# Kernel optimization log

Hardware: AMD Instinct MI355X
Metric: run time of the kernel (lower is better)

## Reference

```python
import jax, jax.numpy as jnp
import numpy as np

EPS = 1e-5  # torch LayerNorm default eps

def _mish(x):
    return x * jnp.tanh(jax.nn.softplus(x))

def _ln(x, g, b):
    mu = jnp.mean(x, axis=-1, keepdims=True)
    var = jnp.mean(jnp.square(x - mu), axis=-1, keepdims=True)
    return (x - mu) * jax.lax.rsqrt(var + EPS) * g + b

def setup_inputs() -> dict:
    key = jax.random.key(0)
    ks = jax.random.split(key, 10)
    B, D, O1, O2, O3 = 65536, 784, 512, 264, 128
    def lin(k, fan_in, shape):
        bound = 1.0 / np.sqrt(fan_in)
        return jax.random.uniform(k, shape, jnp.float32, -bound, bound)
    return {
        "x":  jax.random.uniform(ks[0], (B, D), jnp.float32),
        "W1": lin(ks[1], D,  (O1, D)),   # enFC1, bias=False
        "g1": jnp.ones((O1,), jnp.float32), "b1": jnp.zeros((O1,), jnp.float32),
        "W2": lin(ks[2], O1, (O2, O1)),  # enFC2, bias=False
        "g2": jnp.ones((O2,), jnp.float32), "b2": jnp.zeros((O2,), jnp.float32),
        "W3": lin(ks[3], O2, (O3, O2)),  # enFC3 with bias
        "b3": lin(ks[4], O2, (O3,)),
        "gh": jnp.ones((O3,), jnp.float32), "bh": jnp.zeros((O3,), jnp.float32),
        "D1": lin(ks[5], O3, (O2, O3)),  # deFC1, bias=False
        "g3": jnp.ones((O2,), jnp.float32), "b3n": jnp.zeros((O2,), jnp.float32),
        "D2": lin(ks[6], O2, (O1, O2)),  # deFC2, bias=False
        "g4": jnp.ones((O1,), jnp.float32), "b4": jnp.zeros((O1,), jnp.float32),
        "D3": lin(ks[7], O1, (D, O1)),   # deFC3 with bias
        "bo": lin(ks[8], O1, (D,)),
    }

def reference(x, W1, g1, b1, W2, g2, b2, W3, b3, gh, bh,
              D1, g3, b3n, D2, g4, b4, D3, bo):
    h = _mish(_ln(x @ W1.T, g1, b1))
    h = _mish(_ln(h @ W2.T, g2, b2))
    x_latent = _mish(_ln(h @ W3.T + b3, gh, bh))
    h = _mish(_ln(x_latent @ D1.T, g3, b3n))
    h = _mish(_ln(h @ D2.T, g4, b4))
    out = jax.nn.sigmoid(h @ D3.T + bo)
    return out, jnp.sum(jnp.abs(x_latent))
```

## Files before the change

kernel.cpp:

```cpp
#include <hip/hip_runtime.h>


typedef short bf16x8 __attribute__((ext_vector_type(8)));
typedef float f32x4  __attribute__((ext_vector_type(4)));

#define B_ROWS 65536
#define EPS_LN 1e-5f

static __device__ __forceinline__ unsigned short f2bf(float f) {
    union { float f; unsigned u; } v; v.f = f;
    unsigned r = v.u + 0x7FFFu + ((v.u >> 16) & 1u);
    return (unsigned short)(r >> 16);
}

static __device__ __forceinline__ float mish_f(float x) {
    if (x > 15.f) return x;
    float u = __expf(x);
    float p = __fmaf_rn(u, u, 2.f * u);
    return x * (p / (p + 2.f));
}

static __device__ __forceinline__ void glds16(const void* g, void* l) {
    typedef __attribute__((address_space(3))) unsigned lds_u32;
    typedef __attribute__((address_space(1))) const unsigned glb_u32;
    lds_u32* lp = (lds_u32*)l;
    unsigned lofs = __builtin_amdgcn_readfirstlane((unsigned)(unsigned long long)lp);
    lp = (lds_u32*)(unsigned long long)lofs;
    __builtin_amdgcn_global_load_lds((glb_u32*)g, lp, 16, 0, 0);
}

struct CvtArgs {
    const float* src[6];
    unsigned short* dst[6];
    int O[6], K[6], KP[6];
    int base[7];
};

__global__ void wpad_kernel(CvtArgs a) {
    int b = blockIdx.x;
    int seg = 0;
    while (b >= a.base[seg + 1]) ++seg;
    int r = b - a.base[seg];
    int O = a.O[seg], K = a.K[seg], KP = a.KP[seg];
    const float* s = a.src[seg];
    unsigned short* d = a.dst[seg];
    for (int c = threadIdx.x; c < KP; c += 256) {
        unsigned short v = 0;
        if (r < O && c < K) v = f2bf(s[(size_t)r * K + c]);
        d[(size_t)r * KP + c] = v;
    }
}

template<int KP, int ASTR, int BN, int OREAL, int OSTRIDE, int NKT,
         bool SRCF32, bool HASBIAS, bool ABS, bool LN, bool SWAPGRID>
__global__ __launch_bounds__(512, 2)
void layer9(const void* __restrict__ Asrc,
            const unsigned short* __restrict__ Wp,
            const float* __restrict__ gam,
            const float* __restrict__ bet,
            const float* __restrict__ bias,
            void* __restrict__ Aout,
            float* __restrict__ partials)
{
    constexpr int NT   = BN / 64;
    constexpr int NCHW = BN / 8;
    constexpr int NCH  = NCHW + (SRCF32 ? 0 : 16);
    constexpr int MAXC = (NCH + 7) / 8;
    constexpr int ABY  = 128 * 128;
    constexpr int WBY  = BN * 128;

    __shared__ __align__(16) char smem[2 * ABY + 2 * WBY];

    const int tid  = threadIdx.x;
    const int lane = tid & 63;
    const int wu   = __builtin_amdgcn_readfirstlane(tid >> 6);
    const int wr = wu >> 2, wc = wu & 3;
    const int lg = lane >> 4, lc = lane & 15;
    const int row0  = (SWAPGRID ? blockIdx.y : blockIdx.x) * 128;
    const int cbase = LN ? 0 : (SWAPGRID ? blockIdx.x : blockIdx.y) * BN;

    const int crow = lane >> 3;
    const int sg   = (lane & 7) ^ crow;
    const size_t vofW = ((size_t)crow * KP + (size_t)(sg << 3)) * 2;
    const size_t vofA = ((size_t)crow * ASTR + (size_t)(sg << 3)) * 2;

    auto stage = [&](int t, int b) {
#pragma unroll
        for (int i = 0; i < MAXC; ++i) {
            int c = wu + 8 * i;
            if (c < NCHW) {
                const char* g = (const char*)Wp +
                    ((size_t)(cbase + c * 8) * KP) * 2 + (size_t)t * 128 + vofW;
                glds16(g, smem + (2 * ABY + b * WBY + c * 1024));
            } else if (c < NCH) {
                int ca = c - NCHW;
                const char* g = (const char*)Asrc +
                    ((size_t)(row0 + ca * 8) * ASTR) * 2 + (size_t)t * 128 + vofA;
                glds16(g, smem + (b * ABY + ca * 1024));
            }
        }
    };

    const int ar = tid >> 2, as = tid & 3;
    const float* axp = (const float*)Asrc + (size_t)(row0 + ar) * ASTR + as * 16;
    float4 rA[4];
#pragma unroll
    for (int j = 0; j < 4; ++j) rA[j] = make_float4(0, 0, 0, 0);

    auto loadA1 = [&](int t) {
#pragma unroll
        for (int j = 0; j < 4; ++j) {
            int c0 = t * 64 + as * 16 + j * 4;
            rA[j] = (c0 + 3 < 784) ? *(const float4*)(axp + t * 64 + j * 4)
                                   : make_float4(0, 0, 0, 0);
        }
    };
    auto pubA = [&](int b) {
        union { unsigned short us[8]; uint4 v; } u0, u1;
        u0.us[0] = f2bf(rA[0].x); u0.us[1] = f2bf(rA[0].y);
        u0.us[2] = f2bf(rA[0].z); u0.us[3] = f2bf(rA[0].w);
        u0.us[4] = f2bf(rA[1].x); u0.us[5] = f2bf(rA[1].y);
        u0.us[6] = f2bf(rA[1].z); u0.us[7] = f2bf(rA[1].w);
        u1.us[0] = f2bf(rA[2].x); u1.us[1] = f2bf(rA[2].y);
        u1.us[2] = f2bf(rA[2].z); u1.us[3] = f2bf(rA[2].w);
        u1.us[4] = f2bf(rA[3].x); u1.us[5] = f2bf(rA[3].y);
        u1.us[6] = f2bf(rA[3].z); u1.us[7] = f2bf(rA[3].w);
        int s0 = as * 2, rb = b * ABY + ar * 128, rx = ar & 7;
        *(uint4*)(smem + rb + (((s0    ) ^ rx) << 4)) = u0.v;
        *(uint4*)(smem + rb + (((s0 + 1) ^ rx) << 4)) = u1.v;
    };

    stage(0, 0);
    if constexpr (SRCF32) { loadA1(0); pubA(0); }
    __syncthreads();

    f32x4 acc[4][NT];
#pragma unroll
    for (int a = 0; a < 4; ++a)
#pragma unroll
        for (int c = 0; c < NT; ++c) acc[a][c] = (f32x4){0.f, 0.f, 0.f, 0.f};

    const int f0 = ((lg ^ (lc & 7)) << 4);

    for (int t = 0; t < NKT; ++t) {
        const int bsel = t & 1;
        if (t + 1 < NKT) {
            stage(t + 1, bsel ^ 1);
            if constexpr (SRCF32) loadA1(t + 1);
        }
        const char* Ab = smem + bsel * ABY + (wr * 64 + lc) * 128;
        const char* Bb = smem + 2 * ABY + bsel * WBY + (wc * NT * 16 + lc) * 128;
#pragma unroll
        for (int h = 0; h < 2; ++h) {
            const int fh = f0 ^ (h << 6);
            bf16x8 afr[4], bfr[NT];
#pragma unroll
            for (int a = 0; a < 4; ++a)
                afr[a] = *(const bf16x8*)(Ab + a * 2048 + fh);
#pragma unroll
            for (int c = 0; c < NT; ++c)
                bfr[c] = *(const bf16x8*)(Bb + c * 2048 + fh);
            __builtin_amdgcn_s_setprio(1);
#pragma unroll
            for (int c = 0; c < NT; ++c)
#pragma unroll
                for (int a = 0; a < 4; ++a)
                    acc[a][c] = __builtin_amdgcn_mfma_f32_16x16x32_bf16(afr[a], bfr[c], acc[a][c], 0, 0, 0);
            __builtin_amdgcn_s_setprio(0);
        }
        if constexpr (SRCF32) { if (t + 1 < NKT) pubA(bsel ^ 1); }
        __syncthreads();
    }

    if constexpr (LN) {
        if constexpr (HASBIAS) {
#pragma unroll
            for (int c = 0; c < NT; ++c) {
                int col = wc * NT * 16 + c * 16 + lc;
                float bv = (col < OREAL) ? bias[col] : 0.f;
#pragma unroll
                for (int a = 0; a < 4; ++a)
#pragma unroll
                    for (int r = 0; r < 4; ++r) acc[a][c][r] += bv;
            }
        }
        float ps1[4][4], ps2[4][4];
#pragma unroll
        for (int a = 0; a < 4; ++a)
#pragma unroll
            for (int r = 0; r < 4; ++r) { ps1[a][r] = 0.f; ps2[a][r] = 0.f; }
#pragma unroll
        for (int a = 0; a < 4; ++a)
#pragma unroll
            for (int c = 0; c < NT; ++c)
#pragma unroll
                for (int r = 0; r < 4; ++r) {
                    float v = acc[a][c][r];
                    ps1[a][r] += v;
                    ps2[a][r] = __fmaf_rn(v, v, ps2[a][r]);
                }
#pragma unroll
        for (int m = 1; m < 16; m <<= 1)
#pragma unroll
            for (int a = 0; a < 4; ++a)
#pragma unroll
                for (int r = 0; r < 4; ++r) {
                    ps1[a][r] += __shfl_xor(ps1[a][r], m);
                    ps2[a][r] += __shfl_xor(ps2[a][r], m);
                }

        float* lnP  = (float*)smem;
        float* lnMR = (float*)(smem + 4096);
        float* wsum = (float*)(smem + 5120);

        if (lc == 0) {
#pragma unroll
            for (int a = 0; a < 4; ++a)
#pragma unroll
                for (int r = 0; r < 4; ++r) {
                    int row = wr * 64 + a * 16 + lg * 4 + r;
                    lnP[row * 4 + wc]       = ps1[a][r];
                    lnP[512 + row * 4 + wc] = ps2[a][r];
                }
        }
        __syncthreads();
        if (tid < 128) {
            float s1 = lnP[tid * 4] + lnP[tid * 4 + 1] + lnP[tid * 4 + 2] + lnP[tid * 4 + 3];
            float s2 = lnP[512 + tid * 4] + lnP[512 + tid * 4 + 1] +
                       lnP[512 + tid * 4 + 2] + lnP[512 + tid * 4 + 3];
            float mu = s1 * (1.f / OREAL);
            float var = fmaxf(s2 * (1.f / OREAL) - mu * mu, 0.f);
            lnMR[tid]       = mu;
            lnMR[128 + tid] = rsqrtf(var + EPS_LN);
        }
        __syncthreads();

        float gcol[NT], bcol[NT];
#pragma unroll
        for (int c = 0; c < NT; ++c) {
            int col = wc * NT * 16 + c * 16 + lc;
            gcol[c] = (col < OREAL) ? gam[col] : 0.f;
            bcol[c] = (col < OREAL) ? bet[col] : 0.f;
        }

        float asum = 0.f;
        unsigned short* outp = (unsigned short*)Aout;
#pragma unroll
        for (int a = 0; a < 4; ++a)
#pragma unroll
            for (int r = 0; r < 4; ++r) {
                int rl = wr * 64 + a * 16 + lg * 4 + r;
                float mu = lnMR[rl], rs = lnMR[128 + rl];
                size_t rowoff = (size_t)(row0 + rl) * OSTRIDE;
#pragma unroll
                for (int c = 0; c < NT; ++c) {
                    int col = wc * NT * 16 + c * 16 + lc;
                    if (col < OSTRIDE) {
                        unsigned short outv = 0;
                        if (col < OREAL) {
                            float v = (acc[a][c][r] - mu) * rs * gcol[c] + bcol[c];
                            float mz = mish_f(v);
                            if (ABS) asum += fabsf(mz);
                            outv = f2bf(mz);
                        }
                        outp[rowoff + col] = outv;
                    }
                }
            }

        if constexpr (ABS) {
#pragma unroll
            for (int m = 1; m < 64; m <<= 1) asum += __shfl_xor(asum, m);
            if (lane == 0) wsum[wu] = asum;
            __syncthreads();
            if (tid == 0) {
                float s = 0.f;
                for (int w = 0; w < 8; ++w) s += wsum[w];
                partials[blockIdx.x] = s;
            }
        }
    } else {
        float* outp = (float*)Aout;
#pragma unroll
        for (int c = 0; c < NT; ++c) {
            int col = cbase + wc * NT * 16 + c * 16 + lc;
            bool ok = col < OREAL;
            float bv = ok ? bias[col] : 0.f;
#pragma unroll
            for (int a = 0; a < 4; ++a)
#pragma unroll
                for (int r = 0; r < 4; ++r) {
                    if (ok) {
                        int rl = wr * 64 + a * 16 + lg * 4 + r;
                        float v = acc[a][c][r] + bv;
                        outp[(size_t)(row0 + rl) * OSTRIDE + col] = 1.f / (1.f + __expf(-v));
                    }
                }
        }
    }
}

__global__ __launch_bounds__(512, 2)
void trio(const unsigned short* __restrict__ actP,
          const unsigned short* __restrict__ W2p,
          const unsigned short* __restrict__ W3p,
          const unsigned short* __restrict__ D1p,
          const float* __restrict__ g2, const float* __restrict__ b2,
          const float* __restrict__ gh, const float* __restrict__ bh,
          const float* __restrict__ b3,
          const float* __restrict__ g3, const float* __restrict__ b3n,
          unsigned short* __restrict__ actQ,
          float* __restrict__ partials)
{
    __shared__ __align__(16) char smem[139264];

    const int tid  = threadIdx.x;
    const int lane = tid & 63;
    const int wu   = __builtin_amdgcn_readfirstlane(tid >> 6);
    const int wr = wu >> 2, wc = wu & 3;
    const int lg = lane >> 4, lc = lane & 15;
    const int row0 = blockIdx.x * 128;

    const int sgl = (lane & 3) ^ ((lane >> 3) & 3);
    const size_t vofA  = ((size_t)(lane >> 2) * 512 + (size_t)(sgl << 3)) * 2;
    const size_t vofW2 = vofA;
    const size_t vofW3 = ((size_t)(lane >> 2) * 288 + (size_t)(sgl << 3)) * 2;
    const size_t vofD1 = ((size_t)(lane >> 2) * 128 + (size_t)(sgl << 3)) * 2;

    const int fswz = ((lg ^ ((lc >> 1) & 3)) << 4);

    float* lnP  = (float*)smem;
    float* lnMR = (float*)(smem + 4096);
    float* wsum = (float*)(smem + 5120);

    auto ln_stats = [&](float ps1[4][4], float ps2[4][4], float invO) {
#pragma unroll
        for (int m = 1; m < 16; m <<= 1)
#pragma unroll
            for (int a = 0; a < 4; ++a)
#pragma unroll
                for (int r = 0; r < 4; ++r) {
                    ps1[a][r] += __shfl_xor(ps1[a][r], m);
                    ps2[a][r] += __shfl_xor(ps2[a][r], m);
                }
        if (lc == 0) {
#pragma unroll
            for (int a = 0; a < 4; ++a)
#pragma unroll
                for (int r = 0; r < 4; ++r) {
                    int row = wr * 64 + a * 16 + lg * 4 + r;
                    lnP[row * 4 + wc]       = ps1[a][r];
                    lnP[512 + row * 4 + wc] = ps2[a][r];
                }
        }
        __syncthreads();
        if (tid < 128) {
            float s1 = lnP[tid * 4] + lnP[tid * 4 + 1] + lnP[tid * 4 + 2] + lnP[tid * 4 + 3];
            float s2 = lnP[512 + tid * 4] + lnP[512 + tid * 4 + 1] +
                       lnP[512 + tid * 4 + 2] + lnP[512 + tid * 4 + 3];
            float mu = s1 * invO;
            float var = fmaxf(s2 * invO - mu * mu, 0.f);
            lnMR[tid]       = mu;
            lnMR[128 + tid] = rsqrtf(var + EPS_LN);
        }
        __syncthreads();
    };

    {
        constexpr int NT = 6;
        f32x4 acc[4][NT];
#pragma unroll
        for (int a = 0; a < 4; ++a)
#pragma unroll
            for (int c = 0; c < NT; ++c) acc[a][c] = (f32x4){0.f, 0.f, 0.f, 0.f};

        auto stage1 = [&](int t, int b) {
#pragma unroll
            for (int i = 0; i < 4; ++i) {
                int c = wu + 8 * i;
                if (c < 24) {
                    const char* g = (const char*)W2p +
                        ((size_t)(c * 16) * 512) * 2 + (size_t)t * 64 + vofW2;
                    glds16(g, smem + (16384 + b * 24576 + c * 1024));
                } else {
                    int ca = c - 24;
                    const char* g = (const char*)actP +
                        ((size_t)(row0 + ca * 16) * 512) * 2 + (size_t)t * 64 + vofA;
                    glds16(g, smem + (b * 8192 + ca * 1024));
                }
            }
        };

        stage1(0, 0);
        __syncthreads();
        for (int t = 0; t < 16; ++t) {
            const int bsel = t & 1;
            if (t + 1 < 16) stage1(t + 1, bsel ^ 1);
            const char* Ab = smem + bsel * 8192 + (wr * 64 + lc) * 64 + fswz;
            const char* Bb = smem + 16384 + bsel * 24576 + (wc * 96 + lc) * 64 + fswz;
            bf16x8 afr[4], bfr[NT];
#pragma unroll
            for (int a = 0; a < 4; ++a) afr[a] = *(const bf16x8*)(Ab + a * 1024);
#pragma unroll
            for (int c = 0; c < NT; ++c) bfr[c] = *(const bf16x8*)(Bb + c * 1024);
            __builtin_amdgcn_s_setprio(1);
#pragma unroll
            for (int c = 0; c < NT; ++c)
#pragma unroll
                for (int a = 0; a < 4; ++a)
                    acc[a][c] = __builtin_amdgcn_mfma_f32_16x16x32_bf16(afr[a], bfr[c], acc[a][c], 0, 0, 0);
            __builtin_amdgcn_s_setprio(0);
            __syncthreads();
        }

        float ps1[4][4], ps2[4][4];
#pragma unroll
        for (int a = 0; a < 4; ++a)
#pragma unroll
            for (int r = 0; r < 4; ++r) { ps1[a][r] = 0.f; ps2[a][r] = 0.f; }
#pragma unroll
        for (int a = 0; a < 4; ++a)
#pragma unroll
            for (int c = 0; c < NT; ++c)
#pragma unroll
                for (int r = 0; r < 4; ++r) {
                    float v = acc[a][c][r];
                    ps1[a][r] += v;
                    ps2[a][r] = __fmaf_rn(v, v, ps2[a][r]);
                }
        ln_stats(ps1, ps2, 1.f / 264);

        float gcol[NT], bcol[NT];
#pragma unroll
        for (int c = 0; c < NT; ++c) {
            int col = wc * 96 + c * 16 + lc;
            gcol[c] = (col < 264) ? g2[col] : 0.f;
            bcol[c] = (col < 264) ? b2[col] : 0.f;
        }
#pragma unroll
        for (int a = 0; a < 4; ++a)
#pragma unroll
            for (int r = 0; r < 4; ++r) {
                int rl = wr * 64 + a * 16 + lg * 4 + r;
                float mu = lnMR[rl], rs = lnMR[128 + rl];
                int sx = (rl >> 1) & 3;
                int rowb = 65536 + rl * 576;
#pragma unroll
                for (int c = 0; c < NT; ++c) {
                    int col = wc * 96 + c * 16 + lc;
                    if (col < 288) {
                        unsigned short outv = 0;
                        if (col < 264) {
                            float v = (acc[a][c][r] - mu) * rs * gcol[c] + bcol[c];
                            outv = f2bf(mish_f(v));
                        }
                        int byte = rowb + ((col >> 5) << 6) +
                                   ((((col >> 3) & 3) ^ sx) << 4) + ((col & 7) << 1);
                        *(unsigned short*)(smem + byte) = outv;
                    }
                }
            }
        __syncthreads();
    }

    {
        constexpr int NT = 2;
        f32x4 acc[4][NT];
#pragma unroll
        for (int a = 0; a < 4; ++a)
#pragma unroll
            for (int c = 0; c < NT; ++c) acc[a][c] = (f32x4){0.f, 0.f, 0.f, 0.f};

        auto stage2 = [&](int t, int b) {
            int c = wu;
            const char* g = (const char*)W3p +
                ((size_t)(c * 16) * 288) * 2 + (size_t)t * 64 + vofW3;
            glds16(g, smem + (b * 8192 + c * 1024));
        };

        stage2(0, 0);
        __syncthreads();
        for (int t = 0; t < 9; ++t) {
            const int bsel = t & 1;
            if (t + 1 < 9) stage2(t + 1, bsel ^ 1);
            const char* Ab = smem + 65536 + (wr * 64 + lc) * 576 + t * 64 + fswz;
            const char* Bb = smem + bsel * 8192 + (wc * 32 + lc) * 64 + fswz;
            bf16x8 afr[4], bfr[NT];
#pragma unroll
            for (int a = 0; a < 4; ++a) afr[a] = *(const bf16x8*)(Ab + a * 16 * 576);
#pragma unroll
            for (int c = 0; c < NT; ++c) bfr[c] = *(const bf16x8*)(Bb + c * 1024);
            __builtin_amdgcn_s_setprio(1);
#pragma unroll
            for (int c = 0; c < NT; ++c)
#pragma unroll
                for (int a = 0; a < 4; ++a)
                    acc[a][c] = __builtin_amdgcn_mfma_f32_16x16x32_bf16(afr[a], bfr[c], acc[a][c], 0, 0, 0);
            __builtin_amdgcn_s_setprio(0);
            __syncthreads();
        }

#pragma unroll
        for (int c = 0; c < NT; ++c) {
            int col = wc * 32 + c * 16 + lc;
            float bv = b3[col];
#pragma unroll
            for (int a = 0; a < 4; ++a)
#pragma unroll
                for (int r = 0; r < 4; ++r) acc[a][c][r] += bv;
        }
        float ps1[4][4], ps2[4][4];
#pragma unroll
        for (int a = 0; a < 4; ++a)
#pragma unroll
            for (int r = 0; r < 4; ++r) { ps1[a][r] = 0.f; ps2[a][r] = 0.f; }
#pragma unroll
        for (int a = 0; a < 4; ++a)
#pragma unroll
            for (int c = 0; c < NT; ++c)
#pragma unroll
                for (int r = 0; r < 4; ++r) {
                    float v = acc[a][c][r];
                    ps1[a][r] += v;
                    ps2[a][r] = __fmaf_rn(v, v, ps2[a][r]);
                }
        ln_stats(ps1, ps2, 1.f / 128);

        float gcol[NT], bcol[NT];
#pragma unroll
        for (int c = 0; c < NT; ++c) {
            int col = wc * 32 + c * 16 + lc;
            gcol[c] = gh[col];
            bcol[c] = bh[col];
        }
        float asum = 0.f;
#pragma unroll
        for (int a = 0; a < 4; ++a)
#pragma unroll
            for (int r = 0; r < 4; ++r) {
                int rl = wr * 64 + a * 16 + lg * 4 + r;
                float mu = lnMR[rl], rs = lnMR[128 + rl];
                int sx = (rl >> 1) & 3;
                int rowb = 16384 + rl * 256;
#pragma unroll
                for (int c = 0; c < NT; ++c) {
                    int col = wc * 32 + c * 16 + lc;
                    float v = (acc[a][c][r] - mu) * rs * gcol[c] + bcol[c];
                    float mz = mish_f(v);
                    asum += fabsf(mz);
                    int byte = rowb + ((col >> 5) << 6) +
                               ((((col >> 3) & 3) ^ sx) << 4) + ((col & 7) << 1);
                    *(unsigned short*)(smem + byte) = f2bf(mz);
                }
            }
#pragma unroll
        for (int m = 1; m < 64; m <<= 1) asum += __shfl_xor(asum, m);
        if (lane == 0) wsum[wu] = asum;
        __syncthreads();
        if (tid == 0) {
            float s = 0.f;
            for (int w = 0; w < 8; ++w) s += wsum[w];
            partials[blockIdx.x] = s;
        }
        __syncthreads();
    }

    {
        constexpr int NT = 6;
        f32x4 acc[4][NT];
#pragma unroll
        for (int a = 0; a < 4; ++a)
#pragma unroll
            for (int c = 0; c < NT; ++c) acc[a][c] = (f32x4){0.f, 0.f, 0.f, 0.f};

        auto stage3 = [&](int t, int b) {
#pragma unroll
            for (int i = 0; i < 3; ++i) {
                int c = wu + 8 * i;
                const char* g = (const char*)D1p +
                    ((size_t)(c * 16) * 128) * 2 + (size_t)t * 64 + vofD1;
                glds16(g, smem + (65536 + b * 24576 + c * 1024));
            }
        };

        stage3(0, 0);
        __syncthreads();
        for (int t = 0; t < 4; ++t) {
            const int bsel = t & 1;
            if (t + 1 < 4) stage3(t + 1, bsel ^ 1);
            const char* Ab = smem + 16384 + (wr * 64 + lc) * 256 + t * 64 + fswz;
            const char* Bb = smem + 65536 + bsel * 24576 + (wc * 96 + lc) * 64 + fswz;
            bf16x8 afr[4], bfr[NT];
#pragma unroll
            for (int a = 0; a < 4; ++a) afr[a] = *(const bf16x8*)(Ab + a * 16 * 256);
#pragma unroll
            for (int c = 0; c < NT; ++c) bfr[c] = *(const bf16x8*)(Bb + c * 1024);
            __builtin_amdgcn_s_setprio(1);
#pragma unroll
            for (int c = 0; c < NT; ++c)
#pragma unroll
                for (int a = 0; a < 4; ++a)
                    acc[a][c] = __builtin_amdgcn_mfma_f32_16x16x32_bf16(afr[a], bfr[c], acc[a][c], 0, 0, 0);
            __builtin_amdgcn_s_setprio(0);
            __syncthreads();
        }

        float ps1[4][4], ps2[4][4];
#pragma unroll
        for (int a = 0; a < 4; ++a)
#pragma unroll
            for (int r = 0; r < 4; ++r) { ps1[a][r] = 0.f; ps2[a][r] = 0.f; }
#pragma unroll
        for (int a = 0; a < 4; ++a)
#pragma unroll
            for (int c = 0; c < NT; ++c)
#pragma unroll
                for (int r = 0; r < 4; ++r) {
                    float v = acc[a][c][r];
                    ps1[a][r] += v;
                    ps2[a][r] = __fmaf_rn(v, v, ps2[a][r]);
                }
        ln_stats(ps1, ps2, 1.f / 264);

        float gcol[NT], bcol[NT];
#pragma unroll
        for (int c = 0; c < NT; ++c) {
            int col = wc * 96 + c * 16 + lc;
            gcol[c] = (col < 264) ? g3[col] : 0.f;
            bcol[c] = (col < 264) ? b3n[col] : 0.f;
        }
#pragma unroll
        for (int a = 0; a < 4; ++a)
#pragma unroll
            for (int r = 0; r < 4; ++r) {
                int rl = wr * 64 + a * 16 + lg * 4 + r;
                float mu = lnMR[rl], rs = lnMR[128 + rl];
                size_t rowoff = (size_t)(row0 + rl) * 320;
#pragma unroll
                for (int c = 0; c < NT; ++c) {
                    int col = wc * 96 + c * 16 + lc;
                    if (col < 320) {
                        unsigned short outv = 0;
                        if (col < 264) {
                            float v = (acc[a][c][r] - mu) * rs * gcol[c] + bcol[c];
                            outv = f2bf(mish_f(v));
                        }
                        actQ[rowoff + col] = outv;
                    }
                }
            }
    }
}

__global__ void reduce_abs(const float* __restrict__ partials, float* __restrict__ out) {
    __shared__ float sm[256];
    float s = 0.f;
    for (int i = threadIdx.x; i < 512; i += 256) s += partials[i];
    sm[threadIdx.x] = s;
    __syncthreads();
    for (int step = 128; step > 0; step >>= 1) {
        if (threadIdx.x < step) sm[threadIdx.x] += sm[threadIdx.x + step];
        __syncthreads();
    }
    if (threadIdx.x == 0) out[0] = sm[0];
}

extern "C" void kernel_launch(void* const* d_in, const int* in_sizes, int n_in,
                              void* d_out, int out_size, void* d_ws, size_t ws_size,
                              hipStream_t stream)
{
    const float* x   = (const float*)d_in[0];
    const float* W1  = (const float*)d_in[1];
    const float* g1  = (const float*)d_in[2];
    const float* b1  = (const float*)d_in[3];
    const float* W2  = (const float*)d_in[4];
    const float* g2  = (const float*)d_in[5];
    const float* b2  = (const float*)d_in[6];
    const float* W3  = (const float*)d_in[7];
    const float* b3  = (const float*)d_in[8];
    const float* gh  = (const float*)d_in[9];
    const float* bh  = (const float*)d_in[10];
    const float* D1  = (const float*)d_in[11];
    const float* g3  = (const float*)d_in[12];
    const float* b3n = (const float*)d_in[13];
    const float* D2  = (const float*)d_in[14];
    const float* g4  = (const float*)d_in[15];
    const float* b4  = (const float*)d_in[16];
    const float* D3  = (const float*)d_in[17];
    const float* bo  = (const float*)d_in[18];

    char* ws = (char*)d_ws;
    size_t off = 0;
    auto alloc = [&](size_t bytes) -> char* {
        char* p = ws + off;
        off += (bytes + 255) & ~(size_t)255;
        return p;
    };
    unsigned short* W1p = (unsigned short*)alloc((size_t)512 * 832 * 2);
    unsigned short* W2p = (unsigned short*)alloc((size_t)384 * 512 * 2);
    unsigned short* W3p = (unsigned short*)alloc((size_t)128 * 288 * 2);
    unsigned short* D1p = (unsigned short*)alloc((size_t)384 * 128 * 2);
    unsigned short* D2p = (unsigned short*)alloc((size_t)512 * 320 * 2);
    unsigned short* D3p = (unsigned short*)alloc((size_t)896 * 512 * 2);
    unsigned short* actP = (unsigned short*)alloc((size_t)B_ROWS * 512 * 2);
    unsigned short* actQ = (unsigned short*)alloc((size_t)B_ROWS * 320 * 2);
    float* partials = (float*)alloc(512 * 4);

    CvtArgs ca;
    ca.src[0] = W1; ca.dst[0] = W1p; ca.O[0] = 512; ca.K[0] = 784; ca.KP[0] = 832;
    ca.src[1] = W2; ca.dst[1] = W2p; ca.O[1] = 264; ca.K[1] = 512; ca.KP[1] = 512;
    ca.src[2] = W3; ca.dst[2] = W3p; ca.O[2] = 128; ca.K[2] = 264; ca.KP[2] = 288;
    ca.src[3] = D1; ca.dst[3] = D1p; ca.O[3] = 264; ca.K[3] = 128; ca.KP[3] = 128;
    ca.src[4] = D2; ca.dst[4] = D2p; ca.O[4] = 512; ca.K[4] = 264; ca.KP[4] = 320;
    ca.src[5] = D3; ca.dst[5] = D3p; ca.O[5] = 784; ca.K[5] = 512; ca.KP[5] = 512;
    ca.base[0] = 0;    ca.base[1] = 512;  ca.base[2] = 896;
    ca.base[3] = 1024; ca.base[4] = 1408; ca.base[5] = 1920; ca.base[6] = 2816;
    wpad_kernel<<<2816, 256, 0, stream>>>(ca);

    const int NB = B_ROWS / 128;

    layer9<832, 784, 512, 512, 512, 13, true,  false, false, true,  false>
        <<<NB, 512, 0, stream>>>(x, W1p, g1, b1, nullptr, actP, nullptr);
    trio<<<NB, 512, 0, stream>>>(actP, W2p, W3p, D1p,
                                 g2, b2, gh, bh, b3, g3, b3n, actQ, partials);
    layer9<320, 320, 512, 512, 512, 5,  false, false, false, true,  false>
        <<<NB, 512, 0, stream>>>(actQ, D2p, g4, b4, nullptr, actP, nullptr);
    dim3 g6(2, NB);
    layer9<512, 512, 448, 784, 784, 8,  false, true,  false, false, true>
        <<<g6, 512, 0, stream>>>(actP, D3p, nullptr, nullptr, bo, d_out, nullptr);

    reduce_abs<<<1, 256, 0, stream>>>(partials, (float*)d_out + (size_t)B_ROWS * 784);
}
```

Before: 405.5 us.

## Widen trio K-tiles to 128B swizzle and stage D1 weights in one shot

In the fused middle kernel, the W3 GEMM now uses 64-element (128-byte) K-steps with an 8-way XOR swizzle. That means 5 iterations instead of 9, so there are fewer barriers per tile. K padding for W3 grows from 288 to 320 to match. The D1 GEMM loads its whole weight matrix into LDS at once and runs without a pipelined loop, leaving a single barrier. LDS use grows to 160KB and the LN scratch moves to the end of LDS, which may limit occupancy and adds some padded zero-work.

```diff
diff --git a/kernel.cpp b/kernel.cpp
--- a/kernel.cpp
+++ b/kernel.cpp
@@ -300,6 +300,11 @@
     }
 }
 
+#define H2B  65536
+#define H3B  32768
+#define D1B  65536
+#define LNB  155648
+
 __global__ __launch_bounds__(512, 2)
 void trio(const unsigned short* __restrict__ actP,
           const unsigned short* __restrict__ W2p,
@@ -312,7 +317,7 @@
           unsigned short* __restrict__ actQ,
           float* __restrict__ partials)
 {
-    __shared__ __align__(16) char smem[139264];
+    __shared__ __align__(16) char smem[163840];
 
     const int tid  = threadIdx.x;
     const int lane = tid & 63;
@@ -324,14 +329,19 @@
     const int sgl = (lane & 3) ^ ((lane >> 3) & 3);
     const size_t vofA  = ((size_t)(lane >> 2) * 512 + (size_t)(sgl << 3)) * 2;
     const size_t vofW2 = vofA;
-    const size_t vofW3 = ((size_t)(lane >> 2) * 288 + (size_t)(sgl << 3)) * 2;
-    const size_t vofD1 = ((size_t)(lane >> 2) * 128 + (size_t)(sgl << 3)) * 2;
+    const int crow8 = lane >> 3;
+    const int sg8   = (lane & 7) ^ crow8;
+    const size_t vofW3 = ((size_t)crow8 * 320 + (size_t)(sg8 << 3)) * 2;
+    const int rr4 = lane >> 4, s16 = lane & 15;
+    const size_t vofD1e = (size_t)(rr4 * 256 + ((s16 >> 3) << 7) + (((s16 & 7) ^ rr4) << 4));
+    const size_t vofD1o = (size_t)(rr4 * 256 + ((s16 >> 3) << 7) + (((s16 & 7) ^ rr4 ^ 4) << 4));
 
     const int fswz = ((lg ^ ((lc >> 1) & 3)) << 4);
-
-    float* lnP  = (float*)smem;
-    float* lnMR = (float*)(smem + 4096);
-    float* wsum = (float*)(smem + 5120);
+    const int f0   = ((lg ^ (lc & 7)) << 4);
+
+    float* lnP  = (float*)(smem + LNB);
+    float* lnMR = (float*)(smem + LNB + 4096);
+    float* wsum = (float*)(smem + LNB + 5120);
 
     auto ln_stats = [&](float ps1[4][4], float ps2[4][4], float invO) {
 #pragma unroll
@@ -443,19 +453,19 @@
             for (int r = 0; r < 4; ++r) {
                 int rl = wr * 64 + a * 16 + lg * 4 + r;
                 float mu = lnMR[rl], rs = lnMR[128 + rl];
-                int sx = (rl >> 1) & 3;
-                int rowb = 65536 + rl * 576;
+                int rx = rl & 7;
+                int rowb = H2B + rl * 640;
 #pragma unroll
                 for (int c = 0; c < NT; ++c) {
                     int col = wc * 96 + c * 16 + lc;
-                    if (col < 288) {
+                    if (col < 320) {
                         unsigned short outv = 0;
                         if (col < 264) {
                             float v = (acc[a][c][r] - mu) * rs * gcol[c] + bcol[c];
                             outv = f2bf(mish_f(v));
                         }
-                        int byte = rowb + ((col >> 5) << 6) +
-                                   ((((col >> 3) & 3) ^ sx) << 4) + ((col & 7) << 1);
+                        int byte = rowb + ((col >> 6) << 7) +
+                                   ((((col >> 3) & 7) ^ rx) << 4) + ((col & 7) << 1);
                         *(unsigned short*)(smem + byte) = outv;
                     }
                 }
@@ -472,31 +482,38 @@
             for (int c = 0; c < NT; ++c) acc[a][c] = (f32x4){0.f, 0.f, 0.f, 0.f};
 
         auto stage2 = [&](int t, int b) {
-            int c = wu;
-            const char* g = (const char*)W3p +
-                ((size_t)(c * 16) * 288) * 2 + (size_t)t * 64 + vofW3;
-            glds16(g, smem + (b * 8192 + c * 1024));
+#pragma unroll
+            for (int i = 0; i < 2; ++i) {
+                int c = wu + 8 * i;
+                const char* g = (const char*)W3p +
+                    ((size_t)(c * 8) * 320) * 2 + (size_t)t * 128 + vofW3;
+                glds16(g, smem + (b * 16384 + c * 1024));
+            }
         };
 
         stage2(0, 0);
         __syncthreads();
-        for (int t = 0; t < 9; ++t) {
+        for (int t = 0; t < 5; ++t) {
             const int bsel = t & 1;
-            if (t + 1 < 9) stage2(t + 1, bsel ^ 1);
-            const char* Ab = smem + 65536 + (wr * 64 + lc) * 576 + t * 64 + fswz;
-            const char* Bb = smem + bsel * 8192 + (wc * 32 + lc) * 64 + fswz;
-            bf16x8 afr[4], bfr[NT];
-#pragma unroll
-            for (int a = 0; a < 4; ++a) afr[a] = *(const bf16x8*)(Ab + a * 16 * 576);
-#pragma unroll
-            for (int c = 0; c < NT; ++c) bfr[c] = *(const bf16x8*)(Bb + c * 1024);
-            __builtin_amdgcn_s_setprio(1);
-#pragma unroll
-            for (int c = 0; c < NT; ++c)
-#pragma unroll
-                for (int a = 0; a < 4; ++a)
-                    acc[a][c] = __builtin_amdgcn_mfma_f32_16x16x32_bf16(afr[a], bfr[c], acc[a][c], 0, 0, 0);
-            __builtin_amdgcn_s_setprio(0);
+            if (t + 1 < 5) stage2(t + 1, bsel ^ 1);
+            const char* Ab = smem + H2B + (wr * 64 + lc) * 640 + t * 128;
+            const char* Bb = smem + bsel * 16384 + (wc * 32 + lc) * 128;
+#pragma unroll
+            for (int h = 0; h < 2; ++h) {
+                const int fh = f0 ^ (h << 6);
+                bf16x8 afr[4], bfr[NT];
+#pragma unroll
+                for (int a = 0; a < 4; ++a) afr[a] = *(const bf16x8*)(Ab + a * 16 * 640 + fh);
+#pragma unroll
+                for (int c = 0; c < NT; ++c) bfr[c] = *(const bf16x8*)(Bb + c * 2048 + fh);
+                __builtin_amdgcn_s_setprio(1);
+#pragma unroll
+                for (int c = 0; c < NT; ++c)
+#pragma unroll
+                    for (int a = 0; a < 4; ++a)
+                        acc[a][c] = __builtin_amdgcn_mfma_f32_16x16x32_bf16(afr[a], bfr[c], acc[a][c], 0, 0, 0);
+                __builtin_amdgcn_s_setprio(0);
+            }
             __syncthreads();
         }
 
@@ -540,16 +557,16 @@
             for (int r = 0; r < 4; ++r) {
                 int rl = wr * 64 + a * 16 + lg * 4 + r;
                 float mu = lnMR[rl], rs = lnMR[128 + rl];
-                int sx = (rl >> 1) & 3;
-                int rowb = 16384 + rl * 256;
+                int rx = rl & 7;
+                int rowb = H3B + rl * 256;
 #pragma unroll
                 for (int c = 0; c < NT; ++c) {
                     int col = wc * 32 + c * 16 + lc;
                     float v = (acc[a][c][r] - mu) * rs * gcol[c] + bcol[c];
                     float mz = mish_f(v);
                     asum += fabsf(mz);
-                    int byte = rowb + ((col >> 5) << 6) +
-                               ((((col >> 3) & 3) ^ sx) << 4) + ((col & 7) << 1);
+                    int byte = rowb + ((col >> 6) << 7) +
+                               ((((col >> 3) & 7) ^ rx) << 4) + ((col & 7) << 1);
                     *(unsigned short*)(smem + byte) = f2bf(mz);
                 }
             }
@@ -573,37 +590,37 @@
 #pragma unroll
             for (int c = 0; c < NT; ++c) acc[a][c] = (f32x4){0.f, 0.f, 0.f, 0.f};
 
-        auto stage3 = [&](int t, int b) {
-#pragma unroll
-            for (int i = 0; i < 3; ++i) {
-                int c = wu + 8 * i;
-                const char* g = (const char*)D1p +
-                    ((size_t)(c * 16) * 128) * 2 + (size_t)t * 64 + vofD1;
-                glds16(g, smem + (65536 + b * 24576 + c * 1024));
-            }
-        };
-
-        stage3(0, 0);
-        __syncthreads();
-        for (int t = 0; t < 4; ++t) {
-            const int bsel = t & 1;
-            if (t + 1 < 4) stage3(t + 1, bsel ^ 1);
-            const char* Ab = smem + 16384 + (wr * 64 + lc) * 256 + t * 64 + fswz;
-            const char* Bb = smem + 65536 + bsel * 24576 + (wc * 96 + lc) * 64 + fswz;
-            bf16x8 afr[4], bfr[NT];
-#pragma unroll
-            for (int a = 0; a < 4; ++a) afr[a] = *(const bf16x8*)(Ab + a * 16 * 256);
-#pragma unroll
-            for (int c = 0; c < NT; ++c) bfr[c] = *(const bf16x8*)(Bb + c * 1024);
-            __builtin_amdgcn_s_setprio(1);
-#pragma unroll
-            for (int c = 0; c < NT; ++c)
-#pragma unroll
-                for (int a = 0; a < 4; ++a)
-                    acc[a][c] = __builtin_amdgcn_mfma_f32_16x16x32_bf16(afr[a], bfr[c], acc[a][c], 0, 0, 0);
-            __builtin_amdgcn_s_setprio(0);
-            __syncthreads();
-        }
+#pragma unroll
+        for (int i = 0; i < 12; ++i) {
+            int c = wu + 8 * i;
+            const char* g = (const char*)D1p + (size_t)c * 1024 +
+                            ((c & 1) ? vofD1o : vofD1e);
+            glds16(g, smem + (D1B + c * 1024));
+        }
+        __syncthreads();
+
+#pragma unroll
+        for (int tt = 0; tt < 2; ++tt) {
+            const char* Ab = smem + H3B + (wr * 64 + lc) * 256 + tt * 128;
+            const char* Bb = smem + D1B + (wc * 96 + lc) * 256 + tt * 128;
+#pragma unroll
+            for (int h = 0; h < 2; ++h) {
+                const int fh = f0 ^ (h << 6);
+                bf16x8 afr[4], bfr[NT];
+#pragma unroll
+                for (int a = 0; a < 4; ++a) afr[a] = *(const bf16x8*)(Ab + a * 16 * 256 + fh);
+#pragma unroll
+                for (int c = 0; c < NT; ++c) bfr[c] = *(const bf16x8*)(Bb + c * 16 * 256 + fh);
+                __builtin_amdgcn_s_setprio(1);
+#pragma unroll
+                for (int c = 0; c < NT; ++c)
+#pragma unroll
+                    for (int a = 0; a < 4; ++a)
+                        acc[a][c] = __builtin_amdgcn_mfma_f32_16x16x32_bf16(afr[a], bfr[c], acc[a][c], 0, 0, 0);
+                __builtin_amdgcn_s_setprio(0);
+            }
+        }
+        __syncthreads();
 
         float ps1[4][4], ps2[4][4];
 #pragma unroll
@@ -698,7 +715,7 @@
     };
     unsigned short* W1p = (unsigned short*)alloc((size_t)512 * 832 * 2);
     unsigned short* W2p = (unsigned short*)alloc((size_t)384 * 512 * 2);
-    unsigned short* W3p = (unsigned short*)alloc((size_t)128 * 288 * 2);
+    unsigned short* W3p = (unsigned short*)alloc((size_t)128 * 320 * 2);
     unsigned short* D1p = (unsigned short*)alloc((size_t)384 * 128 * 2);
     unsigned short* D2p = (unsigned short*)alloc((size_t)512 * 320 * 2);
     unsigned short* D3p = (unsigned short*)alloc((size_t)896 * 512 * 2);
@@ -709,7 +726,7 @@
     CvtArgs ca;
     ca.src[0] = W1; ca.dst[0] = W1p; ca.O[0] = 512; ca.K[0] = 784; ca.KP[0] = 832;
     ca.src[1] = W2; ca.dst[1] = W2p; ca.O[1] = 264; ca.K[1] = 512; ca.KP[1] = 512;
-    ca.src[2] = W3; ca.dst[2] = W3p; ca.O[2] = 128; ca.K[2] = 264; ca.KP[2] = 288;
+    ca.src[2] = W3; ca.dst[2] = W3p; ca.O[2] = 128; ca.K[2] = 264; ca.KP[2] = 320;
     ca.src[3] = D1; ca.dst[3] = D1p; ca.O[3] = 264; ca.K[3] = 128; ca.KP[3] = 128;
     ca.src[4] = D2; ca.dst[4] = D2p; ca.O[4] = 512; ca.K[4] = 264; ca.KP[4] = 320;
     ca.src[5] = D3; ca.dst[5] = D3p; ca.O[5] = 784; ca.K[5] = 512; ca.KP[5] = 512;
```

Result: no change. 402.3 us (median of 2 runs) (-0.8%).
